# Performance work log

Hardware: AMD Instinct MI355X
Metric: run time of the kernel (lower is better)

The kernel has to match this reference:

```python
import jax, jax.numpy as jnp
import numpy as np

K = 9        # kernel size
M = 16       # m_max + 1 (angular frequencies, TensorCore-padded)
J = 8        # j_max + 1 (radial Bessel orders, TensorCore-padded)
CIN = 64
COUT = 64
N = 32
H = 64
W = 64


def setup_inputs() -> dict:
    key = jax.random.key(0)
    ks = jax.random.split(key, 6)
    fan_in = CIN * K * K
    x = jax.random.normal(ks[0], (N, CIN, H, W), dtype=jnp.float32)
    # Precomputed complex Bessel-Fourier transition matrix T (constant buffer),
    # shape (M, K*K, J), split into real/imag parts.
    T_real = jax.random.normal(ks[1], (M, K * K, J), dtype=jnp.float32) * 0.1
    T_imag = jax.random.normal(ks[2], (M, K * K, J), dtype=jnp.float32) * 0.1
    # Learnable spectral weights, He-style init scale sqrt(2/fan_in).
    w_scale = np.sqrt(2.0 / fan_in).astype(np.float32)
    w_r = jax.random.normal(ks[3], (M, J, CIN * COUT), dtype=jnp.float32) * w_scale
    w_i = jax.random.normal(ks[4], (M, J, CIN * COUT), dtype=jnp.float32) * w_scale
    # w_i for m=0 is zeroed in the original init
    w_i = w_i.at[0].set(0.0)
    bound = 1.0 / np.sqrt(fan_in)
    b = jax.random.uniform(ks[5], (COUT,), dtype=jnp.float32, minval=-bound, maxval=bound)
    return {"x": x, "T_real": T_real, "T_imag": T_imag, "w_r": w_r, "w_i": w_i, "b": b}


def reference(x, T_real, T_imag, w_r, w_i, b):
    # Complex matmul building the spatial filter bank:
    #   (M, K^2, J) @ (M, J, Cin*Cout) -> (M, K^2, Cin*Cout)
    wr = jnp.matmul(T_real, w_r) - jnp.matmul(T_imag, w_i)
    wi = jnp.matmul(T_real, w_i) + jnp.matmul(T_imag, w_r)
    # einops '[c] m (k1 k2) (b1 b2) -> (c m b2) b1 k1 k2'
    Wf = jnp.stack([wr, wi], axis=0).reshape(2, M, K, K, CIN, COUT)
    Wf = jnp.transpose(Wf, (0, 1, 5, 4, 2, 3)).reshape(2 * M * COUT, CIN, K, K)
    # conv2d, padding='same', stride=1
    y = jax.lax.conv_general_dilated(
        x, Wf, window_strides=(1, 1), padding='SAME',
        dimension_numbers=('NCHW', 'OIHW', 'NCHW'))
    # square (modulus pieces), then sum over (c, m): 'b (c m b1) w h -> b b1 w h'
    n, _, h, w = y.shape
    y = jnp.square(y).reshape(n, 2, M, COUT, h, w).sum(axis=(1, 2))
    # bias add; scale_inv=False -> take the single scale; activation=None
    return y + b[None, :, None, None]
```

## Files before the change

### kernel.cpp

```cpp
#include <hip/hip_runtime.h>
#include <stdint.h>


typedef unsigned short ushort_t;
typedef __attribute__((ext_vector_type(8))) short short8;
typedef __attribute__((ext_vector_type(4))) float float4v;

typedef const void __attribute__((address_space(1)))* gptr_t;
typedef void __attribute__((address_space(3)))* sptr_t;

__device__ __forceinline__ ushort_t f2bf(float f) {
    union { float f; uint32_t u; } v; v.f = f;
    uint32_t u = v.u;
    u += 0x7fffu + ((u >> 16) & 1u);
    return (ushort_t)(u >> 16);
}

__global__ __launch_bounds__(256) void pad_kernel(const float* __restrict__ x,
                                                  ushort_t* __restrict__ xp) {
    __shared__ float lds[64 * 65];
    const int hp  = blockIdx.x;
    const int b   = blockIdx.y;
    const int tid = threadIdx.x;
    const int h   = hp - 4;
    const bool hvalid = (h >= 0 && h < 64);
    if (hvalid) {
        #pragma unroll
        for (int it = 0; it < 16; ++it) {
            int idx = it * 256 + tid;
            int cin = idx >> 6, w = idx & 63;
            lds[w * 65 + cin] = x[((b * 64 + cin) * 64 + h) * 64 + w];
        }
    }
    __syncthreads();
    #pragma unroll
    for (int it = 0; it < 18; ++it) {
        int o = it * 256 + tid;
        int wp = o >> 6, cin = o & 63;
        int w = wp - 4;
        float val = (hvalid && w >= 0 && w < 64) ? lds[w * 65 + cin] : 0.0f;
        xp[((b * 72 + hp) * 72 + wp) * 64 + cin] = f2bf(val);
    }
}

__global__ __launch_bounds__(256) void wf_kernel(const float* __restrict__ Tr,
                                                 const float* __restrict__ Ti,
                                                 const float* __restrict__ wr,
                                                 const float* __restrict__ wi,
                                                 ushort_t* __restrict__ Wfb) {
    __shared__ float lds[64 * 65];
    const int g   = blockIdx.x;
    const int t   = blockIdx.y;
    const int part = g >> 4, m = g & 15;
    const int tid = threadIdx.x;
    #pragma unroll
    for (int it = 0; it < 16; ++it) {
        int cc = it * 256 + tid;
        float acc = 0.f;
        #pragma unroll
        for (int j = 0; j < 8; ++j) {
            float tr  = Tr[(m * 81 + t) * 8 + j];
            float ti  = Ti[(m * 81 + t) * 8 + j];
            float wrv = wr[(m * 8 + j) * 4096 + cc];
            float wiv = wi[(m * 8 + j) * 4096 + cc];
            acc += (part == 0) ? (tr * wrv - ti * wiv) : (tr * wiv + ti * wrv);
        }
        lds[(cc & 63) * 65 + (cc >> 6)] = acc;
    }
    __syncthreads();
    #pragma unroll
    for (int it = 0; it < 16; ++it) {
        int o = it * 256 + tid;
        int cout = o >> 6, cin = o & 63;
        Wfb[(t * 2048 + cout * 32 + g) * 64 + cin] = f2bf(lds[cout * 65 + cin]);
    }
}

__global__ __launch_bounds__(256, 2) void conv_kernel(const ushort_t* __restrict__ xp,
                                                      const ushort_t* __restrict__ Wfb,
                                                      const float* __restrict__ bias,
                                                      float* __restrict__ out) {
    __shared__ alignas(16) ushort_t As[4 * 72 * 64];
    __shared__ alignas(16) ushort_t Bs[2 * 128 * 64];

    const int pt   = blockIdx.x;
    const int ct   = blockIdx.y;
    const int b    = pt >> 4;
    const int h0   = (pt & 15) * 4;
    const int tid  = threadIdx.x;
    const int wv   = tid >> 6;
    const int lane = tid & 63;
    const int wrow = wv >> 1, wcol = wv & 1;
    const int quad = lane >> 4, lr = lane & 15;
    const int lsw  = ((lane & ~7) | ((lane ^ (lane >> 3)) & 7)) * 16;

    float4v acc[8][4];
    #pragma unroll
    for (int i = 0; i < 8; ++i)
        #pragma unroll
        for (int j = 0; j < 4; ++j) {
            float4v z = {0.f, 0.f, 0.f, 0.f};
            acc[i][j] = z;
        }

    const char* xpb  = (const char*)xp;
    const char* wfb0 = (const char*)Wfb + (size_t)(ct * 128) * 128;

    auto stageA = [&](int dy) {
        #pragma unroll
        for (int k2 = 0; k2 < 9; ++k2) {
            const int c  = wv + 4 * k2;
            const int r  = c / 9;
            const int cs = c - 9 * r;
            const char* g = xpb
                + (size_t)((b * 72 + h0 + dy + r) * 72) * 128
                + (size_t)cs * 1024 + (size_t)lsw;
            __builtin_amdgcn_global_load_lds((gptr_t)g,
                (sptr_t)((char*)As + c * 1024), 16, 0, 0);
        }
    };
    auto stageB = [&](int t) {
        const char* base = wfb0 + (size_t)t * 262144;
        char* dst = (char*)Bs + (t & 1) * 16384;
        #pragma unroll
        for (int k2 = 0; k2 < 4; ++k2) {
            const int c2 = wv * 4 + k2;
            __builtin_amdgcn_global_load_lds((gptr_t)(base + (size_t)c2 * 1024 + (size_t)lsw),
                (sptr_t)(dst + c2 * 1024), 16, 0, 0);
        }
    };

    stageA(0);
    stageB(0);

    for (int dy = 0; dy < 9; ++dy) {
        for (int dx = 0; dx < 9; ++dx) {
            const int t = dy * 9 + dx;
            __syncthreads();
            if (t < 80 && dx < 8) stageB(t + 1);

            const ushort_t* Bp = Bs + (t & 1) * 8192;
            const int akey = (lr + dx) & 7;
            const int bkey = lr & 7;
            const int abase = wrow * 2 * 72 + lr + dx;
            #pragma unroll
            for (int kk = 0; kk < 2; ++kk) {
                short8 a[8], bb[4];
                const int aslot = ((kk * 4 + quad) ^ akey) * 8;
                const int bslot = ((kk * 4 + quad) ^ bkey) * 8;
                #pragma unroll
                for (int j = 0; j < 4; ++j)
                    bb[j] = *(const short8*)&Bp[(wcol * 64 + j * 16 + lr) * 64 + bslot];
                #pragma unroll
                for (int i = 0; i < 8; ++i)
                    a[i] = *(const short8*)&As[(abase + (i >> 2) * 72 + (i & 3) * 16) * 64 + aslot];
                #pragma unroll
                for (int i = 0; i < 8; ++i)
                    #pragma unroll
                    for (int j = 0; j < 4; ++j)
                        acc[i][j] = __builtin_amdgcn_mfma_f32_16x16x32_bf16(
                            a[i], bb[j], acc[i][j], 0, 0, 0);
            }

            if (t < 80 && dx == 8) {
                __syncthreads();
                stageA(dy + 1);
                stageB(t + 1);
            }
        }
    }

    const int c0 = ct * 4 + wcol * 2;
    const float b0 = bias[c0], b1 = bias[c0 + 1];
    #pragma unroll
    for (int i = 0; i < 8; ++i) {
        #pragma unroll
        for (int reg = 0; reg < 4; ++reg) {
            float v0 = acc[i][0][reg] * acc[i][0][reg] + acc[i][1][reg] * acc[i][1][reg];
            float v1 = acc[i][2][reg] * acc[i][2][reg] + acc[i][3][reg] * acc[i][3][reg];
            #pragma unroll
            for (int off = 1; off <= 8; off <<= 1) {
                v0 += __shfl_xor(v0, off, 64);
                v1 += __shfl_xor(v1, off, 64);
            }
            if (lr == 0) {
                const int w = (i & 3) * 16 + quad * 4 + reg;
                const int h = h0 + wrow * 2 + (i >> 2);
                out[((b * 64 + c0    ) * 64 + h) * 64 + w] = v0 + b0;
                out[((b * 64 + c0 + 1) * 64 + h) * 64 + w] = v1 + b1;
            }
        }
    }
}

extern "C" void kernel_launch(void* const* d_in, const int* in_sizes, int n_in,
                              void* d_out, int out_size, void* d_ws, size_t ws_size,
                              hipStream_t stream) {
    const float* x    = (const float*)d_in[0];
    const float* Tr   = (const float*)d_in[1];
    const float* Ti   = (const float*)d_in[2];
    const float* wr   = (const float*)d_in[3];
    const float* wi   = (const float*)d_in[4];
    const float* bias = (const float*)d_in[5];
    float* out = (float*)d_out;

    ushort_t* xp  = (ushort_t*)d_ws;
    ushort_t* Wfb = (ushort_t*)((char*)d_ws + 21233664);

    pad_kernel<<<dim3(72, 32), 256, 0, stream>>>(x, xp);
    wf_kernel<<<dim3(32, 81), 256, 0, stream>>>(Tr, Ti, wr, wi, Wfb);
    conv_kernel<<<dim3(512, 16), 256, 0, stream>>>(xp, Wfb, bias, out);
}
```

Baseline: 2.061 ms.

## Load filter fragments directly into registers and double-buffer input rows in LDS

The weight tiles are no longer staged through LDS. Each lane now reads its MFMA B fragments straight from global memory into registers, software-pipelined one half-step ahead. The freed LDS holds a second input-row buffer, so the next dy's rows prefetch while the current ones are used, and the per-tap __syncthreads becomes one per dy. This removes LDS traffic and barriers for B, at the cost of uncoalesced-ish global/L2 loads whose latency is exposed in the inner loop and more registers.

```diff
diff --git a/kernel.cpp b/kernel.cpp
--- a/kernel.cpp
+++ b/kernel.cpp
@@ -80,8 +80,7 @@
                                                       const ushort_t* __restrict__ Wfb,
                                                       const float* __restrict__ bias,
                                                       float* __restrict__ out) {
-    __shared__ alignas(16) ushort_t As[4 * 72 * 64];
-    __shared__ alignas(16) ushort_t Bs[2 * 128 * 64];
+    __shared__ alignas(16) ushort_t As[2 * 4 * 72 * 64];
 
     const int pt   = blockIdx.x;
     const int ct   = blockIdx.y;
@@ -103,10 +102,12 @@
             acc[i][j] = z;
         }
 
-    const char* xpb  = (const char*)xp;
-    const char* wfb0 = (const char*)Wfb + (size_t)(ct * 128) * 128;
+    const char* xpb = (const char*)xp;
+    const char* wfb_w = (const char*)Wfb
+        + (size_t)(ct * 128 + wcol * 64 + lr) * 128 + (size_t)quad * 16;
 
     auto stageA = [&](int dy) {
+        char* dstb = (char*)As + (dy & 1) * 36864;
         #pragma unroll
         for (int k2 = 0; k2 < 9; ++k2) {
             const int c  = wv + 4 * k2;
@@ -116,62 +117,70 @@
                 + (size_t)((b * 72 + h0 + dy + r) * 72) * 128
                 + (size_t)cs * 1024 + (size_t)lsw;
             __builtin_amdgcn_global_load_lds((gptr_t)g,
-                (sptr_t)((char*)As + c * 1024), 16, 0, 0);
+                (sptr_t)(dstb + c * 1024), 16, 0, 0);
         }
     };
-    auto stageB = [&](int t) {
-        const char* base = wfb0 + (size_t)t * 262144;
-        char* dst = (char*)Bs + (t & 1) * 16384;
-        #pragma unroll
-        for (int k2 = 0; k2 < 4; ++k2) {
-            const int c2 = wv * 4 + k2;
-            __builtin_amdgcn_global_load_lds((gptr_t)(base + (size_t)c2 * 1024 + (size_t)lsw),
-                (sptr_t)(dst + c2 * 1024), 16, 0, 0);
-        }
+
+    short8 w0[4], w1[4];
+    auto loadB = [&](const char* tb, int kk, short8* dst) {
+        #pragma unroll
+        for (int j = 0; j < 4; ++j)
+            dst[j] = *(const short8*)(tb + j * 2048 + kk * 64);
     };
 
     stageA(0);
-    stageB(0);
+    loadB(wfb_w, 0, w0);
 
     for (int dy = 0; dy < 9; ++dy) {
+        __syncthreads();
+        if (dy < 8) stageA(dy + 1);
+        const ushort_t* Ab = As + (dy & 1) * 18432;
+        const char* tb = wfb_w + (size_t)(dy * 9) * 262144;
+        #pragma unroll
         for (int dx = 0; dx < 9; ++dx) {
-            const int t = dy * 9 + dx;
-            __syncthreads();
-            if (t < 80 && dx < 8) stageB(t + 1);
-
-            const ushort_t* Bp = Bs + (t & 1) * 8192;
-            const int akey = (lr + dx) & 7;
-            const int bkey = lr & 7;
-            const int abase = wrow * 2 * 72 + lr + dx;
+            loadB(tb, 1, w1);
+
+            const int akey  = (lr + dx) & 7;
+            const int abase = (wrow * 2) * 72 + lr + dx;
+
             #pragma unroll
-            for (int kk = 0; kk < 2; ++kk) {
-                short8 a[8], bb[4];
-                const int aslot = ((kk * 4 + quad) ^ akey) * 8;
-                const int bslot = ((kk * 4 + quad) ^ bkey) * 8;
-                #pragma unroll
-                for (int j = 0; j < 4; ++j)
-                    bb[j] = *(const short8*)&Bp[(wcol * 64 + j * 16 + lr) * 64 + bslot];
-                #pragma unroll
-                for (int i = 0; i < 8; ++i)
-                    a[i] = *(const short8*)&As[(abase + (i >> 2) * 72 + (i & 3) * 16) * 64 + aslot];
-                #pragma unroll
-                for (int i = 0; i < 8; ++i)
+            for (int ih = 0; ih < 2; ++ih) {
+                short8 a[4];
+                #pragma unroll
+                for (int ii = 0; ii < 4; ++ii)
+                    a[ii] = *(const short8*)&Ab[(abase + ih * 72 + ii * 16) * 64
+                                                + (quad ^ akey) * 8];
+                #pragma unroll
+                for (int ii = 0; ii < 4; ++ii)
                     #pragma unroll
                     for (int j = 0; j < 4; ++j)
-                        acc[i][j] = __builtin_amdgcn_mfma_f32_16x16x32_bf16(
-                            a[i], bb[j], acc[i][j], 0, 0, 0);
-            }
-
-            if (t < 80 && dx == 8) {
-                __syncthreads();
-                stageA(dy + 1);
-                stageB(t + 1);
-            }
+                        acc[ih * 4 + ii][j] = __builtin_amdgcn_mfma_f32_16x16x32_bf16(
+                            a[ii], w0[j], acc[ih * 4 + ii][j], 0, 0, 0);
+            }
+
+            if (dy < 8 || dx < 8) loadB(tb + 262144, 0, w0);
+
+            #pragma unroll
+            for (int ih = 0; ih < 2; ++ih) {
+                short8 a[4];
+                #pragma unroll
+                for (int ii = 0; ii < 4; ++ii)
+                    a[ii] = *(const short8*)&Ab[(abase + ih * 72 + ii * 16) * 64
+                                                + ((4 + quad) ^ akey) * 8];
+                #pragma unroll
+                for (int ii = 0; ii < 4; ++ii)
+                    #pragma unroll
+                    for (int j = 0; j < 4; ++j)
+                        acc[ih * 4 + ii][j] = __builtin_amdgcn_mfma_f32_16x16x32_bf16(
+                            a[ii], w1[j], acc[ih * 4 + ii][j], 0, 0, 0);
+            }
+
+            tb += 262144;
         }
     }
 
     const int c0 = ct * 4 + wcol * 2;
-    const float b0 = bias[c0], b1 = bias[c0 + 1];
+    const float bs0 = bias[c0], bs1 = bias[c0 + 1];
     #pragma unroll
     for (int i = 0; i < 8; ++i) {
         #pragma unroll
@@ -186,8 +195,8 @@
             if (lr == 0) {
                 const int w = (i & 3) * 16 + quad * 4 + reg;
                 const int h = h0 + wrow * 2 + (i >> 2);
-                out[((b * 64 + c0    ) * 64 + h) * 64 + w] = v0 + b0;
-                out[((b * 64 + c0 + 1) * 64 + h) * 64 + w] = v1 + b1;
+                out[((b * 64 + c0    ) * 64 + h) * 64 + w] = v0 + bs0;
+                out[((b * 64 + c0 + 1) * 64 + h) * 64 + w] = v1 + bs1;
             }
         }
     }
```

Result: slower. 2.872 ms (+39.4%).

## Use a rolling 5-row input ring buffer and remap blocks for XCD locality

Applied to the files above, without the earlier changes.

Replaces the per-dy full reload of four padded input rows with a 5-slot ring buffer. Only one new row is prefetched per dy, and it is issued at dx==0 alongside the B prefetch, which removes the extra barrier and the stall at the end of each dy. It also linearizes the grid and remaps block IDs so that consecutive blocks on the same XCD share weight tiles, aiming at better L2 reuse. LDS use per block grows by one row (about 9 KB), which could affect occupancy at 2 blocks per CU.

```diff
diff --git a/kernel.cpp b/kernel.cpp
--- a/kernel.cpp
+++ b/kernel.cpp
@@ -80,13 +80,15 @@
                                                       const ushort_t* __restrict__ Wfb,
                                                       const float* __restrict__ bias,
                                                       float* __restrict__ out) {
-    __shared__ alignas(16) ushort_t As[4 * 72 * 64];
+    __shared__ alignas(16) ushort_t As[5 * 72 * 64];
     __shared__ alignas(16) ushort_t Bs[2 * 128 * 64];
 
-    const int pt   = blockIdx.x;
-    const int ct   = blockIdx.y;
-    const int b    = pt >> 4;
-    const int h0   = (pt & 15) * 4;
+    const int bid = blockIdx.x;
+    const int L   = (bid & 7) * 1024 + (bid >> 3);
+    const int ct  = L >> 9;
+    const int pt  = L & 511;
+    const int b   = pt >> 4;
+    const int h0  = (pt & 15) * 4;
     const int tid  = threadIdx.x;
     const int wv   = tid >> 6;
     const int lane = tid & 63;
@@ -106,17 +108,16 @@
     const char* xpb  = (const char*)xp;
     const char* wfb0 = (const char*)Wfb + (size_t)(ct * 128) * 128;
 
-    auto stageA = [&](int dy) {
-        #pragma unroll
-        for (int k2 = 0; k2 < 9; ++k2) {
-            const int c  = wv + 4 * k2;
-            const int r  = c / 9;
-            const int cs = c - 9 * r;
-            const char* g = xpb
-                + (size_t)((b * 72 + h0 + dy + r) * 72) * 128
-                + (size_t)cs * 1024 + (size_t)lsw;
-            __builtin_amdgcn_global_load_lds((gptr_t)g,
-                (sptr_t)((char*)As + c * 1024), 16, 0, 0);
+    auto stageA = [&](int rho) {
+        const int slot = rho >= 10 ? rho - 10 : (rho >= 5 ? rho - 5 : rho);
+        char* dstb = (char*)As + slot * 9216;
+        const char* gb = xpb + (size_t)(b * 72 + h0 + rho) * 9216;
+        #pragma unroll
+        for (int k = 0; k < 3; ++k) {
+            const int cs = wv + 4 * k;
+            if (cs < 9)
+                __builtin_amdgcn_global_load_lds((gptr_t)(gb + (size_t)cs * 1024 + (size_t)lsw),
+                    (sptr_t)(dstb + cs * 1024), 16, 0, 0);
         }
     };
     auto stageB = [&](int t) {
@@ -130,19 +131,24 @@
         }
     };
 
-    stageA(0);
+    stageA(0); stageA(1); stageA(2); stageA(3);
     stageB(0);
 
+    const int bkey = lr & 7;
     for (int dy = 0; dy < 9; ++dy) {
+        const int r0  = dy + wrow * 2;
+        const int r1  = r0 + 1;
+        const int rs0 = r0 >= 10 ? r0 - 10 : (r0 >= 5 ? r0 - 5 : r0);
+        const int rs1 = r1 >= 10 ? r1 - 10 : (r1 >= 5 ? r1 - 5 : r1);
         for (int dx = 0; dx < 9; ++dx) {
             const int t = dy * 9 + dx;
             __syncthreads();
-            if (t < 80 && dx < 8) stageB(t + 1);
+            if (t < 80) stageB(t + 1);
+            if (dx == 0 && dy < 8) stageA(dy + 4);
 
             const ushort_t* Bp = Bs + (t & 1) * 8192;
             const int akey = (lr + dx) & 7;
-            const int bkey = lr & 7;
-            const int abase = wrow * 2 * 72 + lr + dx;
+            const int pxb  = lr + dx;
             #pragma unroll
             for (int kk = 0; kk < 2; ++kk) {
                 short8 a[8], bb[4];
@@ -152,20 +158,16 @@
                 for (int j = 0; j < 4; ++j)
                     bb[j] = *(const short8*)&Bp[(wcol * 64 + j * 16 + lr) * 64 + bslot];
                 #pragma unroll
-                for (int i = 0; i < 8; ++i)
-                    a[i] = *(const short8*)&As[(abase + (i >> 2) * 72 + (i & 3) * 16) * 64 + aslot];
+                for (int i = 0; i < 8; ++i) {
+                    const int rs = (i >> 2) ? rs1 : rs0;
+                    a[i] = *(const short8*)&As[(rs * 72 + pxb + (i & 3) * 16) * 64 + aslot];
+                }
                 #pragma unroll
                 for (int i = 0; i < 8; ++i)
                     #pragma unroll
                     for (int j = 0; j < 4; ++j)
                         acc[i][j] = __builtin_amdgcn_mfma_f32_16x16x32_bf16(
                             a[i], bb[j], acc[i][j], 0, 0, 0);
-            }
-
-            if (t < 80 && dx == 8) {
-                __syncthreads();
-                stageA(dy + 1);
-                stageB(t + 1);
             }
         }
     }
@@ -209,5 +211,5 @@
 
     pad_kernel<<<dim3(72, 32), 256, 0, stream>>>(x, xp);
     wf_kernel<<<dim3(32, 81), 256, 0, stream>>>(Tr, Ti, wr, wi, Wfb);
-    conv_kernel<<<dim3(512, 16), 256, 0, stream>>>(xp, Wfb, bias, out);
-}
+    conv_kernel<<<dim3(8192), 256, 0, stream>>>(xp, Wfb, bias, out);
+}
```

Result: slower. 2.255 ms (+9.4%).
